# Kernel optimization log

Hardware: AMD Instinct MI355X
Metric: run time of the kernel (lower is better)

The kernel has to match this reference:

```python
import jax, jax.numpy as jnp
import numpy as np

HIDDEN = 1024
NUM_HEADS = 16
BATCH = 2
SEQ = 2048


def setup_inputs() -> dict:
    key = jax.random.key(0)
    ks = jax.random.split(key, 5)
    scale = 1.0 / np.sqrt(HIDDEN)
    return {
        "x": jax.random.normal(ks[0], (BATCH, SEQ, HIDDEN), dtype=jnp.float32),
        "W_qkv": jax.random.normal(ks[1], (HIDDEN, 3 * HIDDEN), dtype=jnp.float32) * scale,
        "b_qkv": jax.random.normal(ks[2], (3 * HIDDEN,), dtype=jnp.float32) * 0.02,
        "W_o": jax.random.normal(ks[3], (HIDDEN, HIDDEN), dtype=jnp.float32) * scale,
        "b_o": jax.random.normal(ks[4], (HIDDEN,), dtype=jnp.float32) * 0.02,
    }


def reference(x, W_qkv, b_qkv, W_o, b_o):
    # x: [B, S, H]
    B, S, H = x.shape
    nh = NUM_HEADS
    hs = H // nh
    qkv = jnp.einsum('bsh,hk->bsk', x, W_qkv) + b_qkv  # [B, S, 3H]
    Q, K, V = qkv[..., :H], qkv[..., H:2 * H], qkv[..., 2 * H:]
    # split heads: [B, nh, S, hs]
    Q = Q.reshape(B, S, nh, hs).transpose(0, 2, 1, 3)
    K = K.reshape(B, S, nh, hs).transpose(0, 2, 1, 3)
    V = V.reshape(B, S, nh, hs).transpose(0, 2, 1, 3)
    scores = jnp.einsum('bnqd,bnkd->bnqk', Q, K) / jnp.sqrt(jnp.asarray(hs, x.dtype))
    # NOTE: the original module applies no causal mask despite its name.
    probs = jax.nn.softmax(scores, axis=-1)
    av = jnp.einsum('bnqk,bnkd->bqnd', probs, V)  # [B, S, nh, hs]
    av = av.reshape(B, S, H)
    return jnp.einsum('bsh,ho->bso', av, W_o) + b_o
```

## Files before the change

### kernel.cpp

```cpp
#include <hip/hip_runtime.h>
#include <hip/hip_bf16.h>
#include <stdint.h>

#define HIDDEN 1024
#define NHEAD  16
#define HS     64
#define BATCH  2
#define SEQ    2048
#define MTOT   (BATCH*SEQ)
#define NQKV   (3*HIDDEN)

typedef __hip_bfloat16 bf16;
typedef __attribute__((ext_vector_type(8))) short s16x8;
typedef __attribute__((ext_vector_type(4))) float f32x4;
typedef __attribute__((ext_vector_type(16))) float f32x16;

__device__ __forceinline__ short f2bf(float f) {
  bf16 h = __float2bfloat16(f);
  return *reinterpret_cast<short*>(&h);
}

__device__ __forceinline__ unsigned cvt_pk_bf16(float lo, float hi) {
  unsigned r;
  asm("v_cvt_pk_bf16_f32 %0, %1, %2" : "=v"(r) : "v"(lo), "v"(hi));
  return r;
}

__device__ __forceinline__ int swz(int row, int blk) {
  return (row*8 + (blk ^ (row & 7)))*8;
}

#define GLOAD_LDS(gp, lp) \
  __builtin_amdgcn_global_load_lds((const __attribute__((address_space(1))) void*)(gp), \
                                   (__attribute__((address_space(3))) void*)(lp), 16, 0, 0)

__device__ __forceinline__ int xcd_swz(int orig, int nwg) {
  return (orig & 7)*(nwg >> 3) + (orig >> 3);
}

__global__ void k_cvt_x(const float* __restrict__ x, short* __restrict__ xb, int n8) {
  int i = blockIdx.x*256 + threadIdx.x;
  if (i >= n8) return;
  const f32x4* xv = (const f32x4*)x;
  f32x4 a = xv[2*i], b = xv[2*i+1];
  s16x8 o = { f2bf(a[0]), f2bf(a[1]), f2bf(a[2]), f2bf(a[3]),
              f2bf(b[0]), f2bf(b[1]), f2bf(b[2]), f2bf(b[3]) };
  *(s16x8*)&xb[i*8] = o;
}

__global__ void k_cvt_wT(const float* __restrict__ W, bf16* __restrict__ WT, int K, int N) {
  __shared__ __align__(16) float tile[64][65];
  int n0 = blockIdx.x*64, k0 = blockIdx.y*64;
  int t = threadIdx.x;
  #pragma unroll
  for (int c = 0; c < 4; c++) {
    int s = c*256 + t;
    int r = s >> 4;
    int cc = s & 15;
    f32x4 v = *(const f32x4*)&W[(size_t)(k0 + r)*N + n0 + cc*4];
    tile[r][cc*4+0] = v[0]; tile[r][cc*4+1] = v[1];
    tile[r][cc*4+2] = v[2]; tile[r][cc*4+3] = v[3];
  }
  __syncthreads();
  #pragma unroll
  for (int c = 0; c < 2; c++) {
    int s = c*256 + t;
    int r = s >> 3;
    int cc = s & 7;
    s16x8 o;
    #pragma unroll
    for (int u = 0; u < 8; u++) o[u] = f2bf(tile[cc*8+u][r]);
    *(s16x8*)&WT[(size_t)(n0 + r)*K + k0 + cc*8] = o;
  }
}

template<int OUT_BF16>
__global__ __launch_bounds__(256) void k_gemm(
    const bf16* __restrict__ A, const bf16* __restrict__ BT,
    const float* __restrict__ bias, void* __restrict__ Cout,
    int M, int N, int K)
{
  __shared__ __align__(16) short Asl[128*64];
  __shared__ __align__(16) short Bsl[128*64];
  int t = threadIdx.x;
  int lane = t & 63, w = t >> 6;
  int q = lane & 15, g = lane >> 4;
  int nwg = gridDim.x*gridDim.y;
  int swzid = xcd_swz(blockIdx.y*gridDim.x + blockIdx.x, nwg);
  int bx = swzid % gridDim.x, by = swzid / gridDim.x;
  int row0 = by*128, col0 = bx*128;
  int wr = (w >> 1)*64, wc = (w & 1)*64;

  f32x4 acc[4][4] = {};

  for (int kt = 0; kt < K; kt += 64) {
    __syncthreads();
    #pragma unroll
    for (int c = 0; c < 4; c++) {
      int s = c*256 + t, r = s >> 3, bd = s & 7, bs = bd ^ (r & 7);
      GLOAD_LDS(&A[(size_t)(row0 + r)*K + kt + bs*8], &Asl[s*8]);
      GLOAD_LDS(&BT[(size_t)(col0 + r)*K + kt + bs*8], &Bsl[s*8]);
    }
    __syncthreads();
    #pragma unroll
    for (int kk = 0; kk < 2; kk++) {
      s16x8 af[4], bfr[4];
      #pragma unroll
      for (int i = 0; i < 4; i++) {
        af[i]  = *(const s16x8*)&Asl[swz(wr + i*16 + q, kk*4 + g)];
        bfr[i] = *(const s16x8*)&Bsl[swz(wc + i*16 + q, kk*4 + g)];
      }
      __builtin_amdgcn_s_setprio(1);
      #pragma unroll
      for (int i = 0; i < 4; i++)
        #pragma unroll
        for (int j = 0; j < 4; j++)
          acc[i][j] = __builtin_amdgcn_mfma_f32_16x16x32_bf16(af[i], bfr[j], acc[i][j], 0, 0, 0);
      __builtin_amdgcn_s_setprio(0);
    }
  }
  #pragma unroll
  for (int i = 0; i < 4; i++) {
    #pragma unroll
    for (int j = 0; j < 4; j++) {
      int col = col0 + wc + j*16 + q;
      float bv = bias[col];
      int rowb = row0 + wr + i*16 + g*4;
      #pragma unroll
      for (int r = 0; r < 4; r++) {
        float v = acc[i][j][r] + bv;
        if (OUT_BF16)
          ((bf16*)Cout)[(size_t)(rowb + r)*N + col] = __float2bfloat16(v);
        else
          ((float*)Cout)[(size_t)(rowb + r)*N + col] = v;
      }
    }
  }
}

__global__ void k_repack_v(const bf16* __restrict__ qkv, bf16* __restrict__ Vt) {
  int s0 = blockIdx.x*64;
  int bh = blockIdx.y;
  int b = bh >> 4, h = bh & 15;
  __shared__ __align__(16) short vt[64][68];
  int t = threadIdx.x;
  #pragma unroll
  for (int c = 0; c < 2; c++) {
    int s = c*256 + t, r = s >> 3, bd = s & 7;
    s16x8 v = *(const s16x8*)&qkv[(size_t)(b*SEQ + s0 + r)*NQKV + 2*HIDDEN + h*HS + bd*8];
    #pragma unroll
    for (int u = 0; u < 8; u++) vt[r][bd*8+u] = v[u];
  }
  __syncthreads();
  #pragma unroll
  for (int c = 0; c < 2; c++) {
    int s = c*256 + t, d = s >> 3, bs8 = s & 7;
    s16x8 o;
    #pragma unroll
    for (int u = 0; u < 8; u++) {
      int p = bs8*8 + u;
      int key = (p & ~12) | ((p & 4) << 1) | ((p & 8) >> 1);
      o[u] = vt[key][d];
    }
    *(s16x8*)&Vt[((size_t)(bh*HS + d))*SEQ + s0 + bs8*8] = o;
  }
}

__device__ __forceinline__ void attn_stage(
    const bf16* __restrict__ kbase, const bf16* __restrict__ vbase,
    int kv, int th, short* Ks, short* Vs)
{
  #pragma unroll
  for (int c = 0; c < 2; c++) {
    int s = c*256 + th, r = s >> 3, bd = s & 7, bs = bd ^ (r & 7);
    GLOAD_LDS(&kbase[(size_t)(kv + r)*NQKV + bs*8], &Ks[s*8]);
  }
  #pragma unroll
  for (int c = 0; c < 2; c++) {
    int s = c*256 + th, d = s >> 3, bd = s & 7, bs = bd ^ (d & 7);
    GLOAD_LDS(&vbase[(size_t)d*SEQ + kv + bs*8], &Vs[s*8]);
  }
}

struct AttnState {
  float psum[2];
  f32x16 oacc[2][2];
};

__device__ __forceinline__ void attn_compute(
    const short* Ks, const short* Vs, const s16x8 qf[2][4],
    int ql, int hi, AttnState& st)
{
  const float SC2 = 0.125f*1.44269504f;
  const float CB  = -12.f*1.44269504f;
  #pragma unroll
  for (int kb = 0; kb < 2; kb++) {
    s16x8 ka[4];
    int krow = kb*32 + ql;
    #pragma unroll
    for (int ks = 0; ks < 4; ks++) {
      int ch = (ks*2 + hi) ^ (krow & 7);
      ka[ks] = *(const s16x8*)&Ks[(krow*8 + ch)*8];
    }
    s16x8 vfrag[2][2];
    #pragma unroll
    for (int kq = 0; kq < 2; kq++) {
      #pragma unroll
      for (int db = 0; db < 2; db++) {
        int row = db*32 + ql;
        int ch = (kb*4 + kq*2 + hi) ^ (row & 7);
        vfrag[kq][db] = *(const s16x8*)&Vs[(row*8 + ch)*8];
      }
    }
    #pragma unroll
    for (int qb = 0; qb < 2; qb++) {
      f32x16 sf = {};
      __builtin_amdgcn_s_setprio(1);
      #pragma unroll
      for (int ks = 0; ks < 4; ks++)
        sf = __builtin_amdgcn_mfma_f32_32x32x16_bf16(ka[ks], qf[qb][ks], sf, 0, 0, 0);
      __builtin_amdgcn_s_setprio(0);

      unsigned pkw[8];
      #pragma unroll
      for (int i = 0; i < 8; i++) {
        float p0 = __builtin_amdgcn_exp2f(__builtin_fmaf(sf[2*i],   SC2, CB));
        float p1 = __builtin_amdgcn_exp2f(__builtin_fmaf(sf[2*i+1], SC2, CB));
        st.psum[qb] += p0 + p1;
        pkw[i] = cvt_pk_bf16(p0, p1);
      }

      __builtin_amdgcn_s_setprio(1);
      #pragma unroll
      for (int kq = 0; kq < 2; kq++) {
        union { unsigned u[4]; s16x8 v; } pu;
        pu.u[0] = pkw[kq*4]; pu.u[1] = pkw[kq*4+1];
        pu.u[2] = pkw[kq*4+2]; pu.u[3] = pkw[kq*4+3];
        s16x8 pa = pu.v;
        #pragma unroll
        for (int db = 0; db < 2; db++)
          st.oacc[qb][db] = __builtin_amdgcn_mfma_f32_32x32x16_bf16(pa, vfrag[kq][db], st.oacc[qb][db], 0, 0, 0);
      }
      __builtin_amdgcn_s_setprio(0);
    }
  }
}

__global__ __launch_bounds__(512) void k_attn(
    const bf16* __restrict__ qkv, const bf16* __restrict__ Vt, bf16* __restrict__ av)
{
  __shared__ __align__(16) short smem[8*4096];
  int t = threadIdx.x;
  int lane = t & 63, w = t >> 6;
  int half = t >> 8, th = t & 255, wq = w & 3;
  int ql = lane & 31, hi = lane >> 5;
  int nwg = gridDim.x*gridDim.y;
  int swzid = xcd_swz(blockIdx.y*gridDim.x + blockIdx.x, nwg);
  int qt = swzid & 7, bh = swzid >> 3;
  int b = bh >> 4, h = bh & 15;

  short* Ks0 = &smem[half*16384];
  short* Vs0 = Ks0 + 4096;
  short* Ks1 = Ks0 + 8192;
  short* Vs1 = Ks0 + 12288;

  s16x8 qf[2][4];
  #pragma unroll
  for (int qb = 0; qb < 2; qb++) {
    const bf16* qrow = qkv + (size_t)(b*SEQ + qt*256 + wq*64 + qb*32 + ql)*NQKV + h*HS;
    #pragma unroll
    for (int ks = 0; ks < 4; ks++)
      qf[qb][ks] = *(const s16x8*)&qrow[ks*16 + hi*8];
  }

  AttnState st;
  st.psum[0] = 0.f; st.psum[1] = 0.f;
  st.oacc[0][0] = (f32x16){}; st.oacc[0][1] = (f32x16){};
  st.oacc[1][0] = (f32x16){}; st.oacc[1][1] = (f32x16){};

  const bf16* kbase = qkv + (size_t)(b*SEQ)*NQKV + HIDDEN + h*HS;
  const bf16* vbase = Vt + (size_t)(bh*HS)*SEQ;
  int kv0 = half*1024;

  attn_stage(kbase, vbase, kv0, th, Ks0, Vs0);
  __syncthreads();

  #pragma unroll 1
  for (int tt = 0; tt < 16; tt += 2) {
    if (tt + 1 < 16) attn_stage(kbase, vbase, kv0 + (tt+1)*64, th, Ks1, Vs1);
    attn_compute(Ks0, Vs0, qf, ql, hi, st);
    __syncthreads();
    if (tt + 2 < 16) attn_stage(kbase, vbase, kv0 + (tt+2)*64, th, Ks0, Vs0);
    attn_compute(Ks1, Vs1, qf, ql, hi, st);
    __syncthreads();
  }

  float* combO = (float*)smem;
  float* combP = (float*)&smem[16384];
  #pragma unroll
  for (int qb = 0; qb < 2; qb++) {
    if (half == 1) {
      #pragma unroll
      for (int db = 0; db < 2; db++)
        #pragma unroll
        for (int r = 0; r < 16; r++)
          combO[((wq*2 + db)*16 + r)*64 + lane] = st.oacc[qb][db][r];
      combP[wq*64 + lane] = st.psum[qb];
    }
    __syncthreads();
    if (half == 0) {
      #pragma unroll
      for (int db = 0; db < 2; db++)
        #pragma unroll
        for (int r = 0; r < 16; r++)
          st.oacc[qb][db][r] += combO[((wq*2 + db)*16 + r)*64 + lane];
      st.psum[qb] += combP[wq*64 + lane];
    }
    __syncthreads();
  }

  if (half == 0) {
    float linv[2];
    #pragma unroll
    for (int qb = 0; qb < 2; qb++) {
      float ps = st.psum[qb] + __shfl_xor(st.psum[qb], 32);
      linv[qb] = 1.f/ps;
    }
    #pragma unroll
    for (int qb = 0; qb < 2; qb++) {
      #pragma unroll
      for (int r = 0; r < 16; r++) {
        int qr = (r & 3) + 8*(r >> 2) + 4*hi;
        float lr = __shfl(linv[qb], qr);
        int row = b*SEQ + qt*256 + wq*64 + qb*32 + qr;
        bf16* orow = av + (size_t)row*HIDDEN + h*HS;
        orow[ql]      = __float2bfloat16(st.oacc[qb][0][r]*lr);
        orow[32 + ql] = __float2bfloat16(st.oacc[qb][1][r]*lr);
      }
    }
  }
}

extern "C" void kernel_launch(void* const* d_in, const int* in_sizes, int n_in,
                              void* d_out, int out_size, void* d_ws, size_t ws_size,
                              hipStream_t stream) {
  const float* x    = (const float*)d_in[0];
  const float* Wqkv = (const float*)d_in[1];
  const float* bqkv = (const float*)d_in[2];
  const float* Wo   = (const float*)d_in[3];
  const float* bo   = (const float*)d_in[4];

  char* ws = (char*)d_ws;
  bf16* xb    = (bf16*)(ws);
  bf16* av    = xb;
  bf16* WqkvT = (bf16*)(ws + (8  << 20));
  bf16* WoT   = (bf16*)(ws + (14 << 20));
  bf16* qkv   = (bf16*)(ws + (16 << 20));
  bf16* Vt    = (bf16*)(ws + (40 << 20));

  k_cvt_x<<<dim3(MTOT*HIDDEN/8/256), 256, 0, stream>>>(x, (short*)xb, MTOT*HIDDEN/8);
  k_cvt_wT<<<dim3(NQKV/64, HIDDEN/64), 256, 0, stream>>>(Wqkv, WqkvT, HIDDEN, NQKV);
  k_cvt_wT<<<dim3(HIDDEN/64, HIDDEN/64), 256, 0, stream>>>(Wo, WoT, HIDDEN, HIDDEN);
  k_gemm<1><<<dim3(NQKV/128, MTOT/128), 256, 0, stream>>>(xb, WqkvT, bqkv, qkv, MTOT, NQKV, HIDDEN);
  k_repack_v<<<dim3(SEQ/64, BATCH*NHEAD), 256, 0, stream>>>(qkv, Vt);
  k_attn<<<dim3(SEQ/256, BATCH*NHEAD), 512, 0, stream>>>(qkv, Vt, av);
  k_gemm<0><<<dim3(HIDDEN/128, MTOT/128), 256, 0, stream>>>(av, WoT, bo, d_out, MTOT, HIDDEN, HIDDEN);
}
```

Baseline: 113.5 us.

## Halve attention query tile per block to cut registers and double grid

Each wave now handles 32 query rows instead of 64, so the attention block covers 128 queries and the grid doubles to 512 workgroups. Accumulator and Q-fragment registers are halved and launch_bounds requests 4 blocks per SM to raise occupancy. The split-KV combine is simplified to a single pass with one fewer barrier pair. In exchange, each K/V tile loaded into LDS is reused by half as many queries, doubling K/V traffic from global memory.

Measured after the change: 170.9 us. +50.6%, slower.

```diff
diff --git a/kernel.cpp b/kernel.cpp
--- a/kernel.cpp
+++ b/kernel.cpp
@@ -182,14 +182,9 @@
   }
 }
 
-struct AttnState {
-  float psum[2];
-  f32x16 oacc[2][2];
-};
-
 __device__ __forceinline__ void attn_compute(
-    const short* Ks, const short* Vs, const s16x8 qf[2][4],
-    int ql, int hi, AttnState& st)
+    const short* Ks, const short* Vs, const s16x8 qf[4],
+    int ql, int hi, float& psum, f32x16& oacc0, f32x16& oacc1)
 {
   const float SC2 = 0.125f*1.44269504f;
   const float CB  = -12.f*1.44269504f;
@@ -212,51 +207,47 @@
         vfrag[kq][db] = *(const s16x8*)&Vs[(row*8 + ch)*8];
       }
     }
-    #pragma unroll
-    for (int qb = 0; qb < 2; qb++) {
-      f32x16 sf = {};
-      __builtin_amdgcn_s_setprio(1);
-      #pragma unroll
-      for (int ks = 0; ks < 4; ks++)
-        sf = __builtin_amdgcn_mfma_f32_32x32x16_bf16(ka[ks], qf[qb][ks], sf, 0, 0, 0);
-      __builtin_amdgcn_s_setprio(0);
-
-      unsigned pkw[8];
-      #pragma unroll
-      for (int i = 0; i < 8; i++) {
-        float p0 = __builtin_amdgcn_exp2f(__builtin_fmaf(sf[2*i],   SC2, CB));
-        float p1 = __builtin_amdgcn_exp2f(__builtin_fmaf(sf[2*i+1], SC2, CB));
-        st.psum[qb] += p0 + p1;
-        pkw[i] = cvt_pk_bf16(p0, p1);
-      }
-
-      __builtin_amdgcn_s_setprio(1);
-      #pragma unroll
-      for (int kq = 0; kq < 2; kq++) {
-        union { unsigned u[4]; s16x8 v; } pu;
-        pu.u[0] = pkw[kq*4]; pu.u[1] = pkw[kq*4+1];
-        pu.u[2] = pkw[kq*4+2]; pu.u[3] = pkw[kq*4+3];
-        s16x8 pa = pu.v;
-        #pragma unroll
-        for (int db = 0; db < 2; db++)
-          st.oacc[qb][db] = __builtin_amdgcn_mfma_f32_32x32x16_bf16(pa, vfrag[kq][db], st.oacc[qb][db], 0, 0, 0);
-      }
-      __builtin_amdgcn_s_setprio(0);
-    }
-  }
-}
-
-__global__ __launch_bounds__(512) void k_attn(
+    f32x16 sf = {};
+    __builtin_amdgcn_s_setprio(1);
+    #pragma unroll
+    for (int ks = 0; ks < 4; ks++)
+      sf = __builtin_amdgcn_mfma_f32_32x32x16_bf16(ka[ks], qf[ks], sf, 0, 0, 0);
+    __builtin_amdgcn_s_setprio(0);
+
+    unsigned pkw[8];
+    #pragma unroll
+    for (int i = 0; i < 8; i++) {
+      float p0 = __builtin_amdgcn_exp2f(__builtin_fmaf(sf[2*i],   SC2, CB));
+      float p1 = __builtin_amdgcn_exp2f(__builtin_fmaf(sf[2*i+1], SC2, CB));
+      psum += p0 + p1;
+      pkw[i] = cvt_pk_bf16(p0, p1);
+    }
+
+    __builtin_amdgcn_s_setprio(1);
+    #pragma unroll
+    for (int kq = 0; kq < 2; kq++) {
+      union { unsigned u[4]; s16x8 v; } pu;
+      pu.u[0] = pkw[kq*4]; pu.u[1] = pkw[kq*4+1];
+      pu.u[2] = pkw[kq*4+2]; pu.u[3] = pkw[kq*4+3];
+      s16x8 pa = pu.v;
+      oacc0 = __builtin_amdgcn_mfma_f32_32x32x16_bf16(pa, vfrag[kq][0], oacc0, 0, 0, 0);
+      oacc1 = __builtin_amdgcn_mfma_f32_32x32x16_bf16(pa, vfrag[kq][1], oacc1, 0, 0, 0);
+    }
+    __builtin_amdgcn_s_setprio(0);
+  }
+}
+
+__global__ __launch_bounds__(512, 4) void k_attn(
     const bf16* __restrict__ qkv, const bf16* __restrict__ Vt, bf16* __restrict__ av)
 {
   __shared__ __align__(16) short smem[8*4096];
   int t = threadIdx.x;
   int lane = t & 63, w = t >> 6;
-  int half = t >> 8, th = t & 255, wq = w & 3;
+  int half = w >> 2, th = t & 255, wq = w & 3;
   int ql = lane & 31, hi = lane >> 5;
   int nwg = gridDim.x*gridDim.y;
   int swzid = xcd_swz(blockIdx.y*gridDim.x + blockIdx.x, nwg);
-  int qt = swzid & 7, bh = swzid >> 3;
+  int qt = swzid & 15, bh = swzid >> 4;
   int b = bh >> 4, h = bh & 15;
 
   short* Ks0 = &smem[half*16384];
@@ -264,19 +255,14 @@
   short* Ks1 = Ks0 + 8192;
   short* Vs1 = Ks0 + 12288;
 
-  s16x8 qf[2][4];
-  #pragma unroll
-  for (int qb = 0; qb < 2; qb++) {
-    const bf16* qrow = qkv + (size_t)(b*SEQ + qt*256 + wq*64 + qb*32 + ql)*NQKV + h*HS;
-    #pragma unroll
-    for (int ks = 0; ks < 4; ks++)
-      qf[qb][ks] = *(const s16x8*)&qrow[ks*16 + hi*8];
-  }
-
-  AttnState st;
-  st.psum[0] = 0.f; st.psum[1] = 0.f;
-  st.oacc[0][0] = (f32x16){}; st.oacc[0][1] = (f32x16){};
-  st.oacc[1][0] = (f32x16){}; st.oacc[1][1] = (f32x16){};
+  const bf16* qrow = qkv + (size_t)(b*SEQ + qt*128 + wq*32 + ql)*NQKV + h*HS;
+  s16x8 qf[4];
+  #pragma unroll
+  for (int ks = 0; ks < 4; ks++)
+    qf[ks] = *(const s16x8*)&qrow[ks*16 + hi*8];
+
+  float psum = 0.f;
+  f32x16 oacc0 = {}, oacc1 = {};
 
   const bf16* kbase = qkv + (size_t)(b*SEQ)*NQKV + HIDDEN + h*HS;
   const bf16* vbase = Vt + (size_t)(bh*HS)*SEQ;
@@ -288,55 +274,44 @@
   #pragma unroll 1
   for (int tt = 0; tt < 16; tt += 2) {
     if (tt + 1 < 16) attn_stage(kbase, vbase, kv0 + (tt+1)*64, th, Ks1, Vs1);
-    attn_compute(Ks0, Vs0, qf, ql, hi, st);
+    attn_compute(Ks0, Vs0, qf, ql, hi, psum, oacc0, oacc1);
     __syncthreads();
     if (tt + 2 < 16) attn_stage(kbase, vbase, kv0 + (tt+2)*64, th, Ks0, Vs0);
-    attn_compute(Ks1, Vs1, qf, ql, hi, st);
+    attn_compute(Ks1, Vs1, qf, ql, hi, psum, oacc0, oacc1);
     __syncthreads();
   }
 
   float* combO = (float*)smem;
-  float* combP = (float*)&smem[16384];
-  #pragma unroll
-  for (int qb = 0; qb < 2; qb++) {
-    if (half == 1) {
-      #pragma unroll
-      for (int db = 0; db < 2; db++)
-        #pragma unroll
-        for (int r = 0; r < 16; r++)
-          combO[((wq*2 + db)*16 + r)*64 + lane] = st.oacc[qb][db][r];
-      combP[wq*64 + lane] = st.psum[qb];
-    }
-    __syncthreads();
-    if (half == 0) {
-      #pragma unroll
-      for (int db = 0; db < 2; db++)
-        #pragma unroll
-        for (int r = 0; r < 16; r++)
-          st.oacc[qb][db][r] += combO[((wq*2 + db)*16 + r)*64 + lane];
-      st.psum[qb] += combP[wq*64 + lane];
-    }
-    __syncthreads();
-  }
-
+  float* combP = combO + 4*2*16*64;
+  if (half == 1) {
+    #pragma unroll
+    for (int db = 0; db < 2; db++) {
+      const f32x16& oa = db ? oacc1 : oacc0;
+      #pragma unroll
+      for (int r = 0; r < 16; r++)
+        combO[((wq*2 + db)*16 + r)*64 + lane] = oa[r];
+    }
+    combP[wq*64 + lane] = psum;
+  }
+  __syncthreads();
   if (half == 0) {
-    float linv[2];
-    #pragma unroll
-    for (int qb = 0; qb < 2; qb++) {
-      float ps = st.psum[qb] + __shfl_xor(st.psum[qb], 32);
-      linv[qb] = 1.f/ps;
-    }
-    #pragma unroll
-    for (int qb = 0; qb < 2; qb++) {
-      #pragma unroll
-      for (int r = 0; r < 16; r++) {
-        int qr = (r & 3) + 8*(r >> 2) + 4*hi;
-        float lr = __shfl(linv[qb], qr);
-        int row = b*SEQ + qt*256 + wq*64 + qb*32 + qr;
-        bf16* orow = av + (size_t)row*HIDDEN + h*HS;
-        orow[ql]      = __float2bfloat16(st.oacc[qb][0][r]*lr);
-        orow[32 + ql] = __float2bfloat16(st.oacc[qb][1][r]*lr);
-      }
+    #pragma unroll
+    for (int r = 0; r < 16; r++) {
+      oacc0[r] += combO[((wq*2 + 0)*16 + r)*64 + lane];
+      oacc1[r] += combO[((wq*2 + 1)*16 + r)*64 + lane];
+    }
+    psum += combP[wq*64 + lane];
+
+    float ps = psum + __shfl_xor(psum, 32);
+    float linv = 1.f/ps;
+    #pragma unroll
+    for (int r = 0; r < 16; r++) {
+      int qr = (r & 3) + 8*(r >> 2) + 4*hi;
+      float lr = __shfl(linv, qr);
+      int row = b*SEQ + qt*128 + wq*32 + qr;
+      bf16* orow = av + (size_t)row*HIDDEN + h*HS;
+      orow[ql]      = __float2bfloat16(oacc0[r]*lr);
+      orow[32 + ql] = __float2bfloat16(oacc1[r]*lr);
     }
   }
 }
@@ -363,6 +338,6 @@
   k_cvt_wT<<<dim3(HIDDEN/64, HIDDEN/64), 256, 0, stream>>>(Wo, WoT, HIDDEN, HIDDEN);
   k_gemm<1><<<dim3(NQKV/128, MTOT/128), 256, 0, stream>>>(xb, WqkvT, bqkv, qkv, MTOT, NQKV, HIDDEN);
   k_repack_v<<<dim3(SEQ/64, BATCH*NHEAD), 256, 0, stream>>>(qkv, Vt);
-  k_attn<<<dim3(SEQ/256, BATCH*NHEAD), 512, 0, stream>>>(qkv, Vt, av);
+  k_attn<<<dim3(SEQ/128, BATCH*NHEAD), 512, 0, stream>>>(qkv, Vt, av);
   k_gemm<0><<<dim3(HIDDEN/128, MTOT/128), 256, 0, stream>>>(av, WoT, bo, d_out, MTOT, HIDDEN, HIDDEN);
 }
```
